# Kernel optimization log

Measured on AMD Instinct MI355X. Metric: run time of the kernel, lower is better.

## Reference

```python
import jax, jax.numpy as jnp
import numpy as np

HEADS, FOLD_W, FOLD_H, PW, PH = 4, 2, 2, 2, 2


def setup_inputs() -> dict:
    key = jax.random.key(0)
    ks = jax.random.split(key, 4)
    B, C, W0, H0 = 64, 128, 56, 56
    hd = HEADS * 24  # 96
    return {
        "x": jax.random.normal(ks[0], (B, C, W0, H0), jnp.float32),
        "Wc": jax.random.normal(ks[1], (hd, C), jnp.float32) * 0.05,
        "bc": jnp.zeros((hd,), jnp.float32),
        "Wp": jax.random.normal(ks[2], (hd, C), jnp.float32) * 0.05,
        "bp": jnp.zeros((hd,), jnp.float32),
        "sim_alpha": jnp.ones((1,), jnp.float32),
        "sim_beta": jnp.zeros((1,), jnp.float32),
        "Wo": jax.random.normal(ks[3], (C, hd), jnp.float32) * 0.05,
        "bo": jnp.zeros((C,), jnp.float32),
    }


def _conv1x1(t, W, b):
    return jnp.einsum('oc,bcwh->bowh', W, t) + b[None, :, None, None]


def _forward(x, Wc, bc, Wp, bp, sim_alpha, sim_beta, Wo, bo):
    B, C, W0, H0 = x.shape
    value = _conv1x1(x, Wp, bp)   # [B, e*c, W0, H0]
    q = _conv1x1(x, Wc, bc)
    hd = q.shape[1] // HEADS
    # 'b (e c) w h -> (b e) c w h'
    split = lambda t: t.reshape(B * HEADS, hd, W0, H0)
    value, q = split(value), split(q)
    # fold: 'b c (f1 w) (f2 h) -> (b f1 f2) c w h'
    w2, h2 = W0 // FOLD_W, H0 // FOLD_H
    def fold(t):
        b0 = t.shape[0]
        return (t.reshape(b0, hd, FOLD_W, w2, FOLD_H, h2)
                 .transpose(0, 2, 4, 1, 3, 5)
                 .reshape(b0 * FOLD_W * FOLD_H, hd, w2, h2))
    value, q = fold(value), fold(q)
    b, c, w, h = q.shape
    # adaptive avg pool to (PW, PH): mean over equal blocks
    def adpool(t):
        return t.reshape(b, c, PW, w // PW, PH, h // PH).mean(axis=(3, 5))
    centers = adpool(q).reshape(b, c, PW * PH).transpose(0, 2, 1)          # [b, M, c]
    value_centers = adpool(value).reshape(b, c, PW * PH).transpose(0, 2, 1)
    qf = q.reshape(b, c, w * h).transpose(0, 2, 1)                          # [b, N, c]
    vf = value.reshape(b, c, w * h).transpose(0, 2, 1)
    eps = 1e-12
    cn = centers / jnp.clip(jnp.linalg.norm(centers, axis=-1, keepdims=True), eps)
    xn = qf / jnp.clip(jnp.linalg.norm(qf, axis=-1, keepdims=True), eps)
    sim = jax.nn.sigmoid(sim_beta + sim_alpha * jnp.einsum('bmc,bnc->bmn', cn, xn))  # [b, M, N]
    # hard top-1 assignment over centers axis
    idx = jnp.argmax(sim, axis=1)                                           # [b, N]
    mask = (jnp.arange(sim.shape[1])[None, :, None] == idx[:, None, :])
    sim = sim * mask
    # weighted combine (segment-sum over patches) instead of huge broadcast
    cluster = (jnp.einsum('bmn,bnc->bmc', sim, vf) + value_centers) / (sim.sum(-1, keepdims=True) + 1.0)
    patches = jnp.einsum('bmn,bmc->bnc', sim, cluster)                      # [b, N, c]
    patches = patches.transpose(0, 2, 1).reshape(b, c, w, h)
    # unfold: '(b f1 f2) c w h -> b c (f1 w) (f2 h)'
    patches = (patches.reshape(B * HEADS, FOLD_W, FOLD_H, c, w, h)
                      .transpose(0, 3, 1, 4, 2, 5)
                      .reshape(B * HEADS, c, W0, H0))
    patches = patches.reshape(B, HEADS * c, W0, H0)
    return _conv1x1(patches, Wo, bo)


def reference(x, Wc, bc, Wp, bp, sim_alpha, sim_beta, Wo, bo):
    return _forward(x, Wc, bc, Wp, bp, sim_alpha, sim_beta, Wo, bo)
```

## Files before the change

kernel.cpp:

```cpp
#include <hip/hip_runtime.h>
#include <math.h>

#define CIN 128
#define HD  96
#define SP  3136
#define ROW 56
#define SLAB 1568

__global__ __launch_bounds__(256) void qv_conv(
    const float* __restrict__ x, const float* __restrict__ Wc,
    const float* __restrict__ bc, const float* __restrict__ Wp,
    const float* __restrict__ bp, float* __restrict__ qbuf,
    float* __restrict__ vbuf)
{
  const int st = blockIdx.x % 49;
  const int b  = blockIdx.x / 49;
  const float* xb = x + (size_t)b * CIN * SP + st * 64;

  __shared__ float xs[32][64];
  __shared__ float wl[32][196];

  const int tid = threadIdx.x;
  const int og = tid >> 4;
  const int sg = tid & 15;

  float acc[12][4];
  #pragma unroll
  for (int i = 0; i < 12; ++i) { acc[i][0]=0.f; acc[i][1]=0.f; acc[i][2]=0.f; acc[i][3]=0.f; }

  for (int kt = 0; kt < 4; ++kt) {
    __syncthreads();
    #pragma unroll
    for (int r = 0; r < 2; ++r) {
      int i = tid + r * 256;
      int cc = i >> 4, s4 = i & 15;
      float4 v = *reinterpret_cast<const float4*>(xb + (size_t)(kt*32 + cc) * SP + s4*4);
      *reinterpret_cast<float4*>(&xs[cc][s4*4]) = v;
    }
    #pragma unroll
    for (int r = 0; r < 6; ++r) {
      int i = tid + r * 256;
      int o  = i >> 3, c4 = i & 7;
      const float* wrow = (o < 96) ? (Wc + (size_t)o * CIN) : (Wp + (size_t)(o - 96) * CIN);
      float4 wv = *reinterpret_cast<const float4*>(wrow + kt*32 + c4*4);
      wl[c4*4+0][o] = wv.x; wl[c4*4+1][o] = wv.y;
      wl[c4*4+2][o] = wv.z; wl[c4*4+3][o] = wv.w;
    }
    __syncthreads();
    #pragma unroll
    for (int cc = 0; cc < 32; ++cc) {
      float xv[4];
      *reinterpret_cast<float4*>(xv) = *reinterpret_cast<const float4*>(&xs[cc][sg*4]);
      float wv[12];
      *reinterpret_cast<float4*>(wv + 0) = *reinterpret_cast<const float4*>(&wl[cc][og*12 + 0]);
      *reinterpret_cast<float4*>(wv + 4) = *reinterpret_cast<const float4*>(&wl[cc][og*12 + 4]);
      *reinterpret_cast<float4*>(wv + 8) = *reinterpret_cast<const float4*>(&wl[cc][og*12 + 8]);
      #pragma unroll
      for (int i = 0; i < 12; ++i)
        #pragma unroll
        for (int j = 0; j < 4; ++j)
          acc[i][j] = fmaf(wv[i], xv[j], acc[i][j]);
    }
  }
  #pragma unroll
  for (int i = 0; i < 12; ++i) {
    int o = og * 12 + i;
    float bias; float* dst;
    if (o < 96) { bias = bc[o];      dst = qbuf + ((size_t)b*96 + o      ) * SP + st*64; }
    else        { bias = bp[o - 96]; dst = vbuf + ((size_t)b*96 + (o - 96)) * SP + st*64; }
    float4 v;
    v.x = acc[i][0] + bias; v.y = acc[i][1] + bias;
    v.z = acc[i][2] + bias; v.w = acc[i][3] + bias;
    *reinterpret_cast<float4*>(dst + sg*4) = v;
  }
}

__global__ __launch_bounds__(512, 4) void cluster_k(
    float* qbuf, const float* __restrict__ vbuf,
    const float* __restrict__ alpha_p, const float* __restrict__ beta_p)
{
  const int blk = blockIdx.x;
  const int f1  = blk & 1;
  const int be  = blk >> 1;
  const size_t base = (size_t)be * 24 * SP + (size_t)(f1 * 28) * ROW;
  float* qp = qbuf + base;
  const float* vp = vbuf + base;

  __shared__ double cnd[24][8];
  __shared__ float  sbest[SLAB];
  __shared__ unsigned char ibest[SLAB];
  __shared__ float  clr[8][24];
  __shared__ float  vcr[8][24];
  __shared__ float  dnf[8];

  const int tid  = threadIdx.x;
  const int wid  = tid >> 6;
  const int lane = tid & 63;

  for (int c = wid; c < 24; c += 8) {
    const float* src = qp + (size_t)c * SP;
    double b0=0,b1=0,b2=0,b3=0,b4=0,b5=0,b6=0,b7=0;
    for (int n = lane; n < SLAB; n += 64) {
      const int w = n / 56, h = n - w * 56;
      const int hf = (h >= 28) ? (h - 28) : h;
      const int g  = ((h >= 28) ? 4 : 0) + ((w >= 14) ? 2 : 0) + ((hf >= 14) ? 1 : 0);
      const double val = (double)src[n];
      b0 += (g==0)?val:0.0; b1 += (g==1)?val:0.0;
      b2 += (g==2)?val:0.0; b3 += (g==3)?val:0.0;
      b4 += (g==4)?val:0.0; b5 += (g==5)?val:0.0;
      b6 += (g==6)?val:0.0; b7 += (g==7)?val:0.0;
    }
    #pragma unroll
    for (int m = 32; m >= 1; m >>= 1) {
      b0 += __shfl_xor(b0,m); b1 += __shfl_xor(b1,m);
      b2 += __shfl_xor(b2,m); b3 += __shfl_xor(b3,m);
      b4 += __shfl_xor(b4,m); b5 += __shfl_xor(b5,m);
      b6 += __shfl_xor(b6,m); b7 += __shfl_xor(b7,m);
    }
    if (lane == 0) {
      cnd[c][0]=b0*(1.0/196.0); cnd[c][1]=b1*(1.0/196.0);
      cnd[c][2]=b2*(1.0/196.0); cnd[c][3]=b3*(1.0/196.0);
      cnd[c][4]=b4*(1.0/196.0); cnd[c][5]=b5*(1.0/196.0);
      cnd[c][6]=b6*(1.0/196.0); cnd[c][7]=b7*(1.0/196.0);
    }
  }
  __syncthreads();
  if (tid < 8) {
    double s = 0.0;
    #pragma unroll
    for (int c = 0; c < 24; ++c) { double t = cnd[c][tid]; s += t * t; }
    const double inv = 1.0 / fmax(sqrt(s), 1e-12);
    #pragma unroll
    for (int c = 0; c < 24; ++c) cnd[c][tid] *= inv;
  }
  __syncthreads();

  const double alpha = (double)alpha_p[0];
  const double beta  = (double)beta_p[0];

  for (int n0 = tid; n0 < SLAB; n0 += 512) {
    const int h  = n0 % 56;
    const int gb = (h >= 28) ? 4 : 0;
    double z0=0,z1=0,z2=0,z3=0,nrm=0;
    for (int c = 0; c < 24; ++c) {
      const double qv = (double)qp[(size_t)c * SP + n0];
      z0 += cnd[c][gb+0]*qv; z1 += cnd[c][gb+1]*qv;
      z2 += cnd[c][gb+2]*qv; z3 += cnd[c][gb+3]*qv;
      nrm += qv*qv;
    }
    const double inv = 1.0 / fmax(sqrt(nrm), 1e-12);
    const double v0 = beta + alpha * (z0 * inv);
    const double v1 = beta + alpha * (z1 * inv);
    const double v2 = beta + alpha * (z2 * inv);
    const double v3 = beta + alpha * (z3 * inv);
    double zb = v0; int bi = 0;
    if (v1 > zb) { zb = v1; bi = 1; }
    if (v2 > zb) { zb = v2; bi = 2; }
    if (v3 > zb) { zb = v3; bi = 3; }
    sbest[n0] = (float)(1.0 / (1.0 + exp(-zb)));
    ibest[n0] = (unsigned char)(gb + bi);
  }
  __syncthreads();

  for (int c = wid; c < 24; c += 8) {
    const float* vsrc = vp + (size_t)c * SP;
    float cl0=0,cl1=0,cl2=0,cl3=0,cl4=0,cl5=0,cl6=0,cl7=0;
    float vc0=0,vc1=0,vc2=0,vc3=0,vc4=0,vc5=0,vc6=0,vc7=0;
    float dn0=0,dn1=0,dn2=0,dn3=0,dn4=0,dn5=0,dn6=0,dn7=0;
    for (int n = lane; n < SLAB; n += 64) {
      const int w = n / 56, h = n - w * 56;
      const int hf = (h >= 28) ? (h - 28) : h;
      const int fb = (h >= 28) ? 4 : 0;
      const float v = vsrc[n];
      const float s = sbest[n];
      const int gi = ibest[n];
      const int gm = fb + ((w >= 14) ? 2 : 0) + ((hf >= 14) ? 1 : 0);
      const float sv = s * v;
      cl0 += (gi==0)?sv:0.f; cl1 += (gi==1)?sv:0.f;
      cl2 += (gi==2)?sv:0.f; cl3 += (gi==3)?sv:0.f;
      cl4 += (gi==4)?sv:0.f; cl5 += (gi==5)?sv:0.f;
      cl6 += (gi==6)?sv:0.f; cl7 += (gi==7)?sv:0.f;
      vc0 += (gm==0)?v:0.f;  vc1 += (gm==1)?v:0.f;
      vc2 += (gm==2)?v:0.f;  vc3 += (gm==3)?v:0.f;
      vc4 += (gm==4)?v:0.f;  vc5 += (gm==5)?v:0.f;
      vc6 += (gm==6)?v:0.f;  vc7 += (gm==7)?v:0.f;
      dn0 += (gi==0)?s:0.f;  dn1 += (gi==1)?s:0.f;
      dn2 += (gi==2)?s:0.f;  dn3 += (gi==3)?s:0.f;
      dn4 += (gi==4)?s:0.f;  dn5 += (gi==5)?s:0.f;
      dn6 += (gi==6)?s:0.f;  dn7 += (gi==7)?s:0.f;
    }
    #pragma unroll
    for (int m = 32; m >= 1; m >>= 1) {
      cl0 += __shfl_xor(cl0,m); cl1 += __shfl_xor(cl1,m);
      cl2 += __shfl_xor(cl2,m); cl3 += __shfl_xor(cl3,m);
      cl4 += __shfl_xor(cl4,m); cl5 += __shfl_xor(cl5,m);
      cl6 += __shfl_xor(cl6,m); cl7 += __shfl_xor(cl7,m);
      vc0 += __shfl_xor(vc0,m); vc1 += __shfl_xor(vc1,m);
      vc2 += __shfl_xor(vc2,m); vc3 += __shfl_xor(vc3,m);
      vc4 += __shfl_xor(vc4,m); vc5 += __shfl_xor(vc5,m);
      vc6 += __shfl_xor(vc6,m); vc7 += __shfl_xor(vc7,m);
      dn0 += __shfl_xor(dn0,m); dn1 += __shfl_xor(dn1,m);
      dn2 += __shfl_xor(dn2,m); dn3 += __shfl_xor(dn3,m);
      dn4 += __shfl_xor(dn4,m); dn5 += __shfl_xor(dn5,m);
      dn6 += __shfl_xor(dn6,m); dn7 += __shfl_xor(dn7,m);
    }
    if (lane == 0) {
      clr[0][c]=cl0; clr[1][c]=cl1; clr[2][c]=cl2; clr[3][c]=cl3;
      clr[4][c]=cl4; clr[5][c]=cl5; clr[6][c]=cl6; clr[7][c]=cl7;
      vcr[0][c]=vc0*(1.f/196.f); vcr[1][c]=vc1*(1.f/196.f);
      vcr[2][c]=vc2*(1.f/196.f); vcr[3][c]=vc3*(1.f/196.f);
      vcr[4][c]=vc4*(1.f/196.f); vcr[5][c]=vc5*(1.f/196.f);
      vcr[6][c]=vc6*(1.f/196.f); vcr[7][c]=vc7*(1.f/196.f);
      if (c == 0) {
        dnf[0]=dn0; dnf[1]=dn1; dnf[2]=dn2; dnf[3]=dn3;
        dnf[4]=dn4; dnf[5]=dn5; dnf[6]=dn6; dnf[7]=dn7;
      }
    }
  }
  __syncthreads();

  if (tid < 192) {
    const int g = tid / 24, c = tid - g * 24;
    qp[2 * (size_t)SP + tid] = (clr[g][c] + vcr[g][c]) / (dnf[g] + 1.0f);
  }
  for (int i = tid; i < SLAB; i += 512) {
    qp[i] = sbest[i];
    reinterpret_cast<unsigned int*>(qp + SP)[i] = (unsigned int)ibest[i];
  }
}

__global__ __launch_bounds__(256) void proj_k(
    float* qbuf, const float* __restrict__ Wo)
{
  const int bid = blockIdx.x;
  const int e   = bid & 3;
  const int f1  = (bid >> 2) & 1;
  const int b   = bid >> 3;
  const float* clfg = qbuf + ((size_t)(b*4 + e) * 24 + 2) * SP + (size_t)(f1*28) * ROW;
  float* projb = qbuf + ((size_t)b * 96 + 3 + f1*3) * SP;

  __shared__ float clfs[8][24];
  const int tid = threadIdx.x;
  if (tid < 192) clfs[tid / 24][tid % 24] = clfg[tid];
  __syncthreads();

  const int co = tid & 127;
  const int kh = tid >> 7;
  float wo_r[24];
  #pragma unroll
  for (int c = 0; c < 24; ++c) wo_r[c] = Wo[(size_t)co * HD + e*24 + c];
  #pragma unroll
  for (int t = 0; t < 4; ++t) {
    const int g = kh * 4 + t;
    float s = 0.f;
    #pragma unroll
    for (int c = 0; c < 24; ++c) s = fmaf(wo_r[c], clfs[g][c], s);
    projb[((size_t)e * 8 + g) * 128 + co] = s;
  }
}

__global__ __launch_bounds__(256) void out_k(
    const float* __restrict__ qbuf, const float* __restrict__ bo,
    float* __restrict__ out)
{
  const int bid = blockIdx.x;
  const int b   = bid / 28;
  const int rem = bid % 28;
  const int f1  = rem / 14;
  const int rp  = rem % 14;
  const int n0  = rp * 112;

  __shared__ float  proj_l[4096];
  __shared__ float4 s_l4[112];
  __shared__ unsigned int g_l[112];
  __shared__ float  out_l[56 * 132];

  const int tid = threadIdx.x;

  {
    const float4* pg = reinterpret_cast<const float4*>(
        qbuf + ((size_t)b * 96 + 3 + f1*3) * SP);
    float4* pl = reinterpret_cast<float4*>(proj_l);
    #pragma unroll
    for (int r = 0; r < 4; ++r) pl[tid + r * 256] = pg[tid + r * 256];
  }
  for (int i = tid; i < 112; i += 256) {
    float4 sv; unsigned int gp = 0;
    #pragma unroll
    for (int e = 0; e < 4; ++e) {
      const float* sp = qbuf + ((size_t)(b*4 + e) * 24) * SP + (size_t)(f1*28) * ROW;
      const float sval = sp[n0 + i];
      const unsigned int gv = reinterpret_cast<const unsigned int*>(sp + SP)[n0 + i];
      if (e == 0) sv.x = sval; else if (e == 1) sv.y = sval;
      else if (e == 2) sv.z = sval; else sv.w = sval;
      gp |= (gv & 7u) << (8 * e);
    }
    s_l4[i] = sv; g_l[i] = gp;
  }
  __syncthreads();

  const int cq  = tid & 31;
  const int sub = tid >> 5;
  const float4 bo4 = *reinterpret_cast<const float4*>(bo + cq * 4);
  const float4* pl4 = reinterpret_cast<const float4*>(proj_l);

  for (int chunk = 0; chunk < 2; ++chunk) {
    const int pbase = chunk * 56;
    #pragma unroll
    for (int i = 0; i < 7; ++i) {
      const int pxl = sub * 7 + i;
      const int px  = pbase + pxl;
      const float4 sv = s_l4[px];
      const unsigned int gp = g_l[px];
      float4 acc = bo4;
      {
        const float4 p = pl4[(0*8 + (gp        & 7u)) * 32 + cq];
        acc.x = fmaf(sv.x, p.x, acc.x); acc.y = fmaf(sv.x, p.y, acc.y);
        acc.z = fmaf(sv.x, p.z, acc.z); acc.w = fmaf(sv.x, p.w, acc.w);
      }
      {
        const float4 p = pl4[(1*8 + ((gp >> 8) & 7u)) * 32 + cq];
        acc.x = fmaf(sv.y, p.x, acc.x); acc.y = fmaf(sv.y, p.y, acc.y);
        acc.z = fmaf(sv.y, p.z, acc.z); acc.w = fmaf(sv.y, p.w, acc.w);
      }
      {
        const float4 p = pl4[(2*8 + ((gp >> 16) & 7u)) * 32 + cq];
        acc.x = fmaf(sv.z, p.x, acc.x); acc.y = fmaf(sv.z, p.y, acc.y);
        acc.z = fmaf(sv.z, p.z, acc.z); acc.w = fmaf(sv.z, p.w, acc.w);
      }
      {
        const float4 p = pl4[(3*8 + ((gp >> 24) & 7u)) * 32 + cq];
        acc.x = fmaf(sv.w, p.x, acc.x); acc.y = fmaf(sv.w, p.y, acc.y);
        acc.z = fmaf(sv.w, p.z, acc.z); acc.w = fmaf(sv.w, p.w, acc.w);
      }
      *reinterpret_cast<float4*>(&out_l[pxl * 132 + cq * 4]) = acc;
    }
    __syncthreads();
    for (int t = tid; t < 128 * 56; t += 256) {
      const int co = t / 56, pxl = t - co * 56;
      out[((size_t)b * 128 + co) * SP + (size_t)f1 * SLAB + n0 + pbase + pxl] =
          out_l[pxl * 132 + co];
    }
    __syncthreads();
  }
}

extern "C" void kernel_launch(void* const* d_in, const int* in_sizes, int n_in,
                              void* d_out, int out_size, void* d_ws, size_t ws_size,
                              hipStream_t stream) {
  const float* x  = (const float*)d_in[0];
  const float* Wc = (const float*)d_in[1];
  const float* bc = (const float*)d_in[2];
  const float* Wp = (const float*)d_in[3];
  const float* bp = (const float*)d_in[4];
  const float* sa = (const float*)d_in[5];
  const float* sb = (const float*)d_in[6];
  const float* Wo = (const float*)d_in[7];
  const float* bo = (const float*)d_in[8];
  float* out  = (float*)d_out;
  float* qbuf = (float*)d_ws;
  float* vbuf = out;

  qv_conv<<<dim3(64 * 49), dim3(256), 0, stream>>>(x, Wc, bc, Wp, bp, qbuf, vbuf);
  cluster_k<<<dim3(512), dim3(512), 0, stream>>>(qbuf, vbuf, sa, sb);
  proj_k<<<dim3(512), dim3(256), 0, stream>>>(qbuf, Wo);
  out_k<<<dim3(1792), dim3(256), 0, stream>>>(qbuf, bo, out);
}
```

Before: 265.8 us.

## Restructure qv 1x1 conv to per-wave output split with pre-transposed weights

Adds a small kernel that transposes and concatenates Wc and Wp into a [128][192] buffer stored in the unused tail of the output. The qv conv drops shared-memory staging and barriers: each wave handles 48 output channels for 64 pixels, loads x directly per lane and reads weights as wave-uniform float4 loads (likely scalar or broadcast). This removes LDS traffic and syncs but gives up the register tiling over pixels, so weights are reloaded per channel per wave, and an extra kernel launch is added.

```diff
diff --git a/kernel.cpp b/kernel.cpp
--- a/kernel.cpp
+++ b/kernel.cpp
@@ -7,71 +7,61 @@
 #define ROW 56
 #define SLAB 1568
 
+__global__ __launch_bounds__(256) void wt_k(
+    const float* __restrict__ Wc, const float* __restrict__ Wp,
+    float* __restrict__ Wt)
+{
+  const int idx = blockIdx.x * 256 + threadIdx.x;
+  if (idx >= 128 * 192) return;
+  const int c = idx / 192, o = idx - c * 192;
+  Wt[idx] = (o < 96) ? Wc[(size_t)o * CIN + c] : Wp[(size_t)(o - 96) * CIN + c];
+}
+
 __global__ __launch_bounds__(256) void qv_conv(
-    const float* __restrict__ x, const float* __restrict__ Wc,
-    const float* __restrict__ bc, const float* __restrict__ Wp,
-    const float* __restrict__ bp, float* __restrict__ qbuf,
-    float* __restrict__ vbuf)
+    const float* __restrict__ x, const float* __restrict__ Wt,
+    const float* __restrict__ bc, const float* __restrict__ bp,
+    float* __restrict__ qbuf, float* __restrict__ vbuf)
 {
   const int st = blockIdx.x % 49;
   const int b  = blockIdx.x / 49;
-  const float* xb = x + (size_t)b * CIN * SP + st * 64;
-
-  __shared__ float xs[32][64];
-  __shared__ float wl[32][196];
-
   const int tid = threadIdx.x;
-  const int og = tid >> 4;
-  const int sg = tid & 15;
-
-  float acc[12][4];
+  const int lane = tid & 63;
+  const int wq = __builtin_amdgcn_readfirstlane(tid >> 6);
+  const float* xg = x + (size_t)b * CIN * SP + st * 64 + lane;
+  const float* wbase = Wt + wq * 48;
+
+  float acc[48];
   #pragma unroll
-  for (int i = 0; i < 12; ++i) { acc[i][0]=0.f; acc[i][1]=0.f; acc[i][2]=0.f; acc[i][3]=0.f; }
-
-  for (int kt = 0; kt < 4; ++kt) {
-    __syncthreads();
-    #pragma unroll
-    for (int r = 0; r < 2; ++r) {
-      int i = tid + r * 256;
-      int cc = i >> 4, s4 = i & 15;
-      float4 v = *reinterpret_cast<const float4*>(xb + (size_t)(kt*32 + cc) * SP + s4*4);
-      *reinterpret_cast<float4*>(&xs[cc][s4*4]) = v;
-    }
-    #pragma unroll
-    for (int r = 0; r < 6; ++r) {
-      int i = tid + r * 256;
-      int o  = i >> 3, c4 = i & 7;
-      const float* wrow = (o < 96) ? (Wc + (size_t)o * CIN) : (Wp + (size_t)(o - 96) * CIN);
-      float4 wv = *reinterpret_cast<const float4*>(wrow + kt*32 + c4*4);
-      wl[c4*4+0][o] = wv.x; wl[c4*4+1][o] = wv.y;
-      wl[c4*4+2][o] = wv.z; wl[c4*4+3][o] = wv.w;
-    }
-    __syncthreads();
-    #pragma unroll
-    for (int cc = 0; cc < 32; ++cc) {
-      float xv[4];
-      *reinterpret_cast<float4*>(xv) = *reinterpret_cast<const float4*>(&xs[cc][sg*4]);
-      float wv[12];
-      *reinterpret_cast<float4*>(wv + 0) = *reinterpret_cast<const float4*>(&wl[cc][og*12 + 0]);
-      *reinterpret_cast<float4*>(wv + 4) = *reinterpret_cast<const float4*>(&wl[cc][og*12 + 4]);
-      *reinterpret_cast<float4*>(wv + 8) = *reinterpret_cast<const float4*>(&wl[cc][og*12 + 8]);
-      #pragma unroll
-      for (int i = 0; i < 12; ++i)
-        #pragma unroll
-        for (int j = 0; j < 4; ++j)
-          acc[i][j] = fmaf(wv[i], xv[j], acc[i][j]);
-    }
-  }
-  #pragma unroll
-  for (int i = 0; i < 12; ++i) {
-    int o = og * 12 + i;
-    float bias; float* dst;
-    if (o < 96) { bias = bc[o];      dst = qbuf + ((size_t)b*96 + o      ) * SP + st*64; }
-    else        { bias = bp[o - 96]; dst = vbuf + ((size_t)b*96 + (o - 96)) * SP + st*64; }
-    float4 v;
-    v.x = acc[i][0] + bias; v.y = acc[i][1] + bias;
-    v.z = acc[i][2] + bias; v.w = acc[i][3] + bias;
-    *reinterpret_cast<float4*>(dst + sg*4) = v;
+  for (int i = 0; i < 48; ++i) acc[i] = 0.f;
+
+  #pragma unroll 2
+  for (int c = 0; c < CIN; ++c) {
+    const float xv = xg[(size_t)c * SP];
+    const float4* wr = reinterpret_cast<const float4*>(wbase + (size_t)c * 192);
+    #pragma unroll
+    for (int j = 0; j < 12; ++j) {
+      const float4 w4 = wr[j];
+      acc[j*4+0] = fmaf(w4.x, xv, acc[j*4+0]);
+      acc[j*4+1] = fmaf(w4.y, xv, acc[j*4+1]);
+      acc[j*4+2] = fmaf(w4.z, xv, acc[j*4+2]);
+      acc[j*4+3] = fmaf(w4.w, xv, acc[j*4+3]);
+    }
+  }
+
+  if (wq < 2) {
+    const int o0 = wq * 48;
+    #pragma unroll
+    for (int i = 0; i < 48; ++i) {
+      const int o = o0 + i;
+      qbuf[((size_t)b * 96 + o) * SP + st * 64 + lane] = acc[i] + bc[o];
+    }
+  } else {
+    const int o0 = wq * 48 - 96;
+    #pragma unroll
+    for (int i = 0; i < 48; ++i) {
+      const int o = o0 + i;
+      vbuf[((size_t)b * 96 + o) * SP + st * 64 + lane] = acc[i] + bp[o];
+    }
   }
 }
 
@@ -360,8 +350,10 @@
   float* out  = (float*)d_out;
   float* qbuf = (float*)d_ws;
   float* vbuf = out;
-
-  qv_conv<<<dim3(64 * 49), dim3(256), 0, stream>>>(x, Wc, bc, Wp, bp, qbuf, vbuf);
+  float* wt   = out + (size_t)64 * 96 * SP;
+
+  wt_k<<<dim3(96), dim3(256), 0, stream>>>(Wc, Wp, wt);
+  qv_conv<<<dim3(64 * 49), dim3(256), 0, stream>>>(x, wt, bc, bp, qbuf, vbuf);
   cluster_k<<<dim3(512), dim3(512), 0, stream>>>(qbuf, vbuf, sa, sb);
   proj_k<<<dim3(512), dim3(256), 0, stream>>>(qbuf, Wo);
   out_k<<<dim3(1792), dim3(256), 0, stream>>>(qbuf, bo, out);
```

Measured after the change: 264.6 us. No clear change (-0.5%).

## Eliminate value conv by folding Wp into output projection and segment-summing x

Applied to the files above, without the earlier changes.

The value 1x1 conv is no longer materialised. Cluster sums are computed directly on x through per-cluster index lists built with ballot compaction and via block means, then projected by a precomputed Wo·Wp matrix plus a bias term. This halves the conv GEMM work and drops the vbuf write and read. It adds a gather-based seg_k kernel with irregular x loads, a larger proj_k GEMM over 128 channels, and a tiny pe_k launch, and it uses the output buffer as scratch for P.

```diff
diff --git a/kernel.cpp b/kernel.cpp
--- a/kernel.cpp
+++ b/kernel.cpp
@@ -7,18 +7,45 @@
 #define ROW 56
 #define SLAB 1568
 
-__global__ __launch_bounds__(256) void qv_conv(
+__global__ __launch_bounds__(256) void pe_k(
+    const float* __restrict__ Wo, const float* __restrict__ Wp,
+    const float* __restrict__ bp, float* __restrict__ P, float* __restrict__ obp)
+{
+  const int e = blockIdx.x;
+  __shared__ float ws[24][128];
+  const int tid = threadIdx.x;
+  for (int i = tid; i < 24 * 128; i += 256)
+    ws[i >> 7][i & 127] = Wp[(size_t)(e * 24 + (i >> 7)) * CIN + (i & 127)];
+  __syncthreads();
+  const int co = tid & 127;
+  const int cig = tid >> 7;
+  float wo_r[24];
+  #pragma unroll
+  for (int c = 0; c < 24; ++c) wo_r[c] = Wo[(size_t)co * HD + e * 24 + c];
+  for (int ci = cig * 64; ci < cig * 64 + 64; ++ci) {
+    float s = 0.f;
+    #pragma unroll
+    for (int c = 0; c < 24; ++c) s = fmaf(wo_r[c], ws[c][ci], s);
+    P[((size_t)e * 128 + ci) * 128 + co] = s;
+  }
+  if (cig == 0) {
+    float s = 0.f;
+    #pragma unroll
+    for (int c = 0; c < 24; ++c) s = fmaf(wo_r[c], bp[e * 24 + c], s);
+    obp[e * 128 + co] = s;
+  }
+}
+
+__global__ __launch_bounds__(128) void q_conv(
     const float* __restrict__ x, const float* __restrict__ Wc,
-    const float* __restrict__ bc, const float* __restrict__ Wp,
-    const float* __restrict__ bp, float* __restrict__ qbuf,
-    float* __restrict__ vbuf)
+    const float* __restrict__ bc, float* __restrict__ qbuf)
 {
   const int st = blockIdx.x % 49;
   const int b  = blockIdx.x / 49;
   const float* xb = x + (size_t)b * CIN * SP + st * 64;
 
   __shared__ float xs[32][64];
-  __shared__ float wl[32][196];
+  __shared__ float wl[32][100];
 
   const int tid = threadIdx.x;
   const int og = tid >> 4;
@@ -31,18 +58,17 @@
   for (int kt = 0; kt < 4; ++kt) {
     __syncthreads();
     #pragma unroll
-    for (int r = 0; r < 2; ++r) {
-      int i = tid + r * 256;
+    for (int r = 0; r < 4; ++r) {
+      int i = tid + r * 128;
       int cc = i >> 4, s4 = i & 15;
       float4 v = *reinterpret_cast<const float4*>(xb + (size_t)(kt*32 + cc) * SP + s4*4);
       *reinterpret_cast<float4*>(&xs[cc][s4*4]) = v;
     }
     #pragma unroll
     for (int r = 0; r < 6; ++r) {
-      int i = tid + r * 256;
+      int i = tid + r * 128;
       int o  = i >> 3, c4 = i & 7;
-      const float* wrow = (o < 96) ? (Wc + (size_t)o * CIN) : (Wp + (size_t)(o - 96) * CIN);
-      float4 wv = *reinterpret_cast<const float4*>(wrow + kt*32 + c4*4);
+      float4 wv = *reinterpret_cast<const float4*>(Wc + (size_t)o * CIN + kt*32 + c4*4);
       wl[c4*4+0][o] = wv.x; wl[c4*4+1][o] = wv.y;
       wl[c4*4+2][o] = wv.z; wl[c4*4+3][o] = wv.w;
     }
@@ -64,34 +90,31 @@
   }
   #pragma unroll
   for (int i = 0; i < 12; ++i) {
-    int o = og * 12 + i;
-    float bias; float* dst;
-    if (o < 96) { bias = bc[o];      dst = qbuf + ((size_t)b*96 + o      ) * SP + st*64; }
-    else        { bias = bp[o - 96]; dst = vbuf + ((size_t)b*96 + (o - 96)) * SP + st*64; }
+    const int o = og * 12 + i;
+    const float bias = bc[o];
     float4 v;
     v.x = acc[i][0] + bias; v.y = acc[i][1] + bias;
     v.z = acc[i][2] + bias; v.w = acc[i][3] + bias;
-    *reinterpret_cast<float4*>(dst + sg*4) = v;
+    *reinterpret_cast<float4*>(qbuf + ((size_t)b*96 + o) * SP + st*64 + sg*4) = v;
   }
 }
 
 __global__ __launch_bounds__(512, 4) void cluster_k(
-    float* qbuf, const float* __restrict__ vbuf,
-    const float* __restrict__ alpha_p, const float* __restrict__ beta_p)
+    float* qbuf, const float* __restrict__ alpha_p, const float* __restrict__ beta_p)
 {
   const int blk = blockIdx.x;
   const int f1  = blk & 1;
   const int be  = blk >> 1;
   const size_t base = (size_t)be * 24 * SP + (size_t)(f1 * 28) * ROW;
   float* qp = qbuf + base;
-  const float* vp = vbuf + base;
 
   __shared__ double cnd[24][8];
   __shared__ float  sbest[SLAB];
   __shared__ unsigned char ibest[SLAB];
-  __shared__ float  clr[8][24];
-  __shared__ float  vcr[8][24];
-  __shared__ float  dnf[8];
+  __shared__ unsigned short nlist[SLAB];
+  __shared__ int   cnts[8];
+  __shared__ int   starts[9];
+  __shared__ float dnl[8];
 
   const int tid  = threadIdx.x;
   const int wid  = tid >> 6;
@@ -162,100 +185,148 @@
   }
   __syncthreads();
 
-  for (int c = wid; c < 24; c += 8) {
-    const float* vsrc = vp + (size_t)c * SP;
-    float cl0=0,cl1=0,cl2=0,cl3=0,cl4=0,cl5=0,cl6=0,cl7=0;
-    float vc0=0,vc1=0,vc2=0,vc3=0,vc4=0,vc5=0,vc6=0,vc7=0;
-    float dn0=0,dn1=0,dn2=0,dn3=0,dn4=0,dn5=0,dn6=0,dn7=0;
-    for (int n = lane; n < SLAB; n += 64) {
-      const int w = n / 56, h = n - w * 56;
-      const int hf = (h >= 28) ? (h - 28) : h;
-      const int fb = (h >= 28) ? 4 : 0;
-      const float v = vsrc[n];
-      const float s = sbest[n];
-      const int gi = ibest[n];
-      const int gm = fb + ((w >= 14) ? 2 : 0) + ((hf >= 14) ? 1 : 0);
-      const float sv = s * v;
-      cl0 += (gi==0)?sv:0.f; cl1 += (gi==1)?sv:0.f;
-      cl2 += (gi==2)?sv:0.f; cl3 += (gi==3)?sv:0.f;
-      cl4 += (gi==4)?sv:0.f; cl5 += (gi==5)?sv:0.f;
-      cl6 += (gi==6)?sv:0.f; cl7 += (gi==7)?sv:0.f;
-      vc0 += (gm==0)?v:0.f;  vc1 += (gm==1)?v:0.f;
-      vc2 += (gm==2)?v:0.f;  vc3 += (gm==3)?v:0.f;
-      vc4 += (gm==4)?v:0.f;  vc5 += (gm==5)?v:0.f;
-      vc6 += (gm==6)?v:0.f;  vc7 += (gm==7)?v:0.f;
-      dn0 += (gi==0)?s:0.f;  dn1 += (gi==1)?s:0.f;
-      dn2 += (gi==2)?s:0.f;  dn3 += (gi==3)?s:0.f;
-      dn4 += (gi==4)?s:0.f;  dn5 += (gi==5)?s:0.f;
-      dn6 += (gi==6)?s:0.f;  dn7 += (gi==7)?s:0.f;
-    }
-    #pragma unroll
-    for (int m = 32; m >= 1; m >>= 1) {
-      cl0 += __shfl_xor(cl0,m); cl1 += __shfl_xor(cl1,m);
-      cl2 += __shfl_xor(cl2,m); cl3 += __shfl_xor(cl3,m);
-      cl4 += __shfl_xor(cl4,m); cl5 += __shfl_xor(cl5,m);
-      cl6 += __shfl_xor(cl6,m); cl7 += __shfl_xor(cl7,m);
-      vc0 += __shfl_xor(vc0,m); vc1 += __shfl_xor(vc1,m);
-      vc2 += __shfl_xor(vc2,m); vc3 += __shfl_xor(vc3,m);
-      vc4 += __shfl_xor(vc4,m); vc5 += __shfl_xor(vc5,m);
-      vc6 += __shfl_xor(vc6,m); vc7 += __shfl_xor(vc7,m);
-      dn0 += __shfl_xor(dn0,m); dn1 += __shfl_xor(dn1,m);
-      dn2 += __shfl_xor(dn2,m); dn3 += __shfl_xor(dn3,m);
-      dn4 += __shfl_xor(dn4,m); dn5 += __shfl_xor(dn5,m);
-      dn6 += __shfl_xor(dn6,m); dn7 += __shfl_xor(dn7,m);
-    }
-    if (lane == 0) {
-      clr[0][c]=cl0; clr[1][c]=cl1; clr[2][c]=cl2; clr[3][c]=cl3;
-      clr[4][c]=cl4; clr[5][c]=cl5; clr[6][c]=cl6; clr[7][c]=cl7;
-      vcr[0][c]=vc0*(1.f/196.f); vcr[1][c]=vc1*(1.f/196.f);
-      vcr[2][c]=vc2*(1.f/196.f); vcr[3][c]=vc3*(1.f/196.f);
-      vcr[4][c]=vc4*(1.f/196.f); vcr[5][c]=vc5*(1.f/196.f);
-      vcr[6][c]=vc6*(1.f/196.f); vcr[7][c]=vc7*(1.f/196.f);
-      if (c == 0) {
-        dnf[0]=dn0; dnf[1]=dn1; dnf[2]=dn2; dnf[3]=dn3;
-        dnf[4]=dn4; dnf[5]=dn5; dnf[6]=dn6; dnf[7]=dn7;
-      }
-    }
-  }
-  __syncthreads();
-
-  if (tid < 192) {
-    const int g = tid / 24, c = tid - g * 24;
-    qp[2 * (size_t)SP + tid] = (clr[g][c] + vcr[g][c]) / (dnf[g] + 1.0f);
-  }
+  if (wid < 8) {
+    float dn = 0.f; int cnt = 0;
+    for (int ch = 0; ch < 25; ++ch) {
+      const int n = ch * 64 + lane;
+      const bool p = (n < SLAB) && (ibest[n] == (unsigned char)wid);
+      const unsigned long long m = __ballot(p);
+      cnt += (int)__popcll(m);
+      dn += p ? sbest[n] : 0.f;
+    }
+    #pragma unroll
+    for (int m = 32; m >= 1; m >>= 1) dn += __shfl_xor(dn, m);
+    if (lane == 0) { cnts[wid] = cnt; dnl[wid] = dn; }
+  }
+  __syncthreads();
+  if (tid == 0) {
+    int a = 0;
+    #pragma unroll
+    for (int k = 0; k < 8; ++k) { starts[k] = a; a += cnts[k]; }
+    starts[8] = a;
+  }
+  __syncthreads();
+  if (wid < 8) {
+    int off = starts[wid];
+    for (int ch = 0; ch < 25; ++ch) {
+      const int n = ch * 64 + lane;
+      const bool p = (n < SLAB) && (ibest[n] == (unsigned char)wid);
+      const unsigned long long m = __ballot(p);
+      if (p) {
+        const int pos = off + (int)__popcll(m & ((1ull << lane) - 1ull));
+        nlist[pos] = (unsigned short)n;
+      }
+      off += (int)__popcll(m);
+    }
+  }
+  __syncthreads();
+
   for (int i = tid; i < SLAB; i += 512) {
     qp[i] = sbest[i];
     reinterpret_cast<unsigned int*>(qp + SP)[i] = (unsigned int)ibest[i];
   }
+  unsigned int* ch2 = reinterpret_cast<unsigned int*>(qp + 2 * (size_t)SP);
+  for (int i = tid; i < 784; i += 512)
+    ch2[i] = (unsigned int)nlist[2*i] | ((unsigned int)nlist[2*i+1] << 16);
+  if (tid < 9) ch2[784 + tid] = (unsigned int)starts[tid];
+  if (tid < 8) reinterpret_cast<float*>(ch2)[800 + tid] = dnl[tid];
+}
+
+__global__ __launch_bounds__(320) void seg_k(
+    float* qbuf, const float* __restrict__ x)
+{
+  const int bid = blockIdx.x;
+  const int b   = bid >> 2;
+  const int f1  = (bid >> 1) & 1;
+  const int c0  = (bid & 1) * 64;
+
+  __shared__ float        s_all[4][SLAB];
+  __shared__ unsigned int nl32[4][784];
+  __shared__ int          st_l[4][9];
+  __shared__ float        inv_l[4][8];
+  __shared__ float        yl[40][64];
+
+  const int tid = threadIdx.x;
+
+  for (int e = 0; e < 4; ++e) {
+    const float* qp = qbuf + (size_t)(b*4 + e) * 24 * SP + (size_t)(f1*28) * ROW;
+    for (int i = tid; i < SLAB; i += 320) s_all[e][i] = qp[i];
+    const unsigned int* ch2 = reinterpret_cast<const unsigned int*>(qp + 2 * (size_t)SP);
+    for (int i = tid; i < 784; i += 320) nl32[e][i] = ch2[i];
+    if (tid < 9) st_l[e][tid] = (int)ch2[784 + tid];
+    if (tid < 8) inv_l[e][tid] = 1.f / (reinterpret_cast<const float*>(ch2)[800 + tid] + 1.f);
+  }
+  __syncthreads();
+
+  const int grp = tid >> 3;
+  const int l8  = tid & 7;
+  const bool dyn = grp < 32;
+  int e = 0, g = 0, i0 = 0, cnt = 0;
+  if (dyn) { e = grp >> 3; g = grp & 7; i0 = st_l[e][g]; cnt = st_l[e][g+1] - i0; }
+  else     { g = grp - 32; cnt = 196; }
+
+  const float* xbase = x + (size_t)b * CIN * SP + (size_t)f1 * SLAB;
+  for (int cl = 0; cl < 64; ++cl) {
+    const float* xc = xbase + (size_t)(c0 + cl) * SP;
+    float s = 0.f;
+    if (dyn) {
+      for (int i = l8; i < cnt; i += 8) {
+        const int idx = i0 + i;
+        const int n = (int)((nl32[e][idx >> 1] >> ((idx & 1) * 16)) & 0xFFFFu);
+        s = fmaf(s_all[e][n], xc[n], s);
+      }
+    } else {
+      const int nb = ((g >> 1) & 1) * 14 * 56 + (g >> 2) * 28 + (g & 1) * 14;
+      for (int i = l8; i < 196; i += 8) {
+        const int wl_ = i / 14, hl = i - wl_ * 14;
+        s += xc[nb + wl_ * 56 + hl];
+      }
+    }
+    s += __shfl_xor(s, 1); s += __shfl_xor(s, 2); s += __shfl_xor(s, 4);
+    if (l8 == 0) yl[grp][cl] = s;
+  }
+  __syncthreads();
+
+  float* yout = qbuf + ((size_t)b * 96 + 9 + f1 * 3) * SP;
+  for (int k = tid; k < 32 * 64; k += 320) {
+    const int eg = k >> 6, cl = k & 63;
+    const int e2 = eg >> 3, g2 = eg & 7;
+    yout[eg * 128 + c0 + cl] =
+        (yl[eg][cl] + yl[32 + g2][cl] * (1.f / 196.f)) * inv_l[e2][g2];
+  }
 }
 
 __global__ __launch_bounds__(256) void proj_k(
-    float* qbuf, const float* __restrict__ Wo)
+    float* qbuf, const float* __restrict__ P, const float* __restrict__ obp)
 {
   const int bid = blockIdx.x;
-  const int e   = bid & 3;
-  const int f1  = (bid >> 2) & 1;
-  const int b   = bid >> 3;
-  const float* clfg = qbuf + ((size_t)(b*4 + e) * 24 + 2) * SP + (size_t)(f1*28) * ROW;
-  float* projb = qbuf + ((size_t)b * 96 + 3 + f1*3) * SP;
-
-  __shared__ float clfs[8][24];
+  const int b = bid >> 1, f1 = bid & 1;
+  __shared__ float ylds[32][128];
   const int tid = threadIdx.x;
-  if (tid < 192) clfs[tid / 24][tid % 24] = clfg[tid];
+  const float* yin = qbuf + ((size_t)b * 96 + 9 + f1 * 3) * SP;
+  for (int i = tid; i < 32 * 128; i += 256) ylds[i >> 7][i & 127] = yin[i];
   __syncthreads();
 
   const int co = tid & 127;
-  const int kh = tid >> 7;
-  float wo_r[24];
+  const int e0 = (tid >> 7) * 2;
+  float a0[8], a1[8];
+  const float o0 = obp[e0 * 128 + co], o1 = obp[(e0 + 1) * 128 + co];
   #pragma unroll
-  for (int c = 0; c < 24; ++c) wo_r[c] = Wo[(size_t)co * HD + e*24 + c];
+  for (int g = 0; g < 8; ++g) { a0[g] = o0; a1[g] = o1; }
+  for (int ci = 0; ci < 128; ++ci) {
+    const float p0 = P[((size_t)e0 * 128 + ci) * 128 + co];
+    const float p1 = P[((size_t)(e0 + 1) * 128 + ci) * 128 + co];
+    #pragma unroll
+    for (int g = 0; g < 8; ++g) {
+      a0[g] = fmaf(p0, ylds[e0 * 8 + g][ci], a0[g]);
+      a1[g] = fmaf(p1, ylds[(e0 + 1) * 8 + g][ci], a1[g]);
+    }
+  }
+  float* pout = qbuf + ((size_t)b * 96 + 3 + f1 * 3) * SP;
   #pragma unroll
-  for (int t = 0; t < 4; ++t) {
-    const int g = kh * 4 + t;
-    float s = 0.f;
-    #pragma unroll
-    for (int c = 0; c < 24; ++c) s = fmaf(wo_r[c], clfs[g][c], s);
-    projb[((size_t)e * 8 + g) * 128 + co] = s;
+  for (int g = 0; g < 8; ++g) {
+    pout[(e0 * 8 + g) * 128 + co]       = a0[g];
+    pout[((e0 + 1) * 8 + g) * 128 + co] = a1[g];
   }
 }
 
@@ -359,10 +430,13 @@
   const float* bo = (const float*)d_in[8];
   float* out  = (float*)d_out;
   float* qbuf = (float*)d_ws;
-  float* vbuf = out;
-
-  qv_conv<<<dim3(64 * 49), dim3(256), 0, stream>>>(x, Wc, bc, Wp, bp, qbuf, vbuf);
-  cluster_k<<<dim3(512), dim3(512), 0, stream>>>(qbuf, vbuf, sa, sb);
-  proj_k<<<dim3(512), dim3(256), 0, stream>>>(qbuf, Wo);
-  out_k<<<dim3(1792), dim3(256), 0, stream>>>(qbuf, bo, out);
-}
+  float* Pbuf = out;
+  float* obpb = out + 65536;
+
+  pe_k   <<<dim3(4),       dim3(256), 0, stream>>>(Wo, Wp, bp, Pbuf, obpb);
+  q_conv <<<dim3(64 * 49), dim3(128), 0, stream>>>(x, Wc, bc, qbuf);
+  cluster_k<<<dim3(512),   dim3(512), 0, stream>>>(qbuf, sa, sb);
+  seg_k  <<<dim3(256),     dim3(320), 0, stream>>>(qbuf, x);
+  proj_k <<<dim3(128),     dim3(256), 0, stream>>>(qbuf, Pbuf, obpb);
+  out_k  <<<dim3(1792),    dim3(256), 0, stream>>>(qbuf, bo, out);
+}
```

Measured after the change: 662.3 us. 2.49x slower.
